# Kernel tuning notes

Hardware: AMD Instinct MI355X
Metric: run time of the kernel (lower is better)

Reference implementation:

```python
import jax, jax.numpy as jnp
import numpy as np

VOCAB = 50257
B, T, D = 32, 2048, 512


def setup_inputs() -> dict:
    key = jax.random.key(0)
    k1, k2, k3 = jax.random.split(key, 3)
    vector_sequence = jax.random.normal(k1, (B, T, D), dtype=jnp.float32)
    # lengths in [1, T] to match realistic sentence lengths (avoids 0/0 in y)
    sentence_length = jax.random.randint(k2, (B,), 1, T + 1, dtype=jnp.int32)
    word_sequence = jax.random.randint(k3, (B, T), 0, VOCAB, dtype=jnp.int32)
    # ParameterDict of scalars flattened to one vector, init = 1/num_of_vocab
    weights = jnp.ones((VOCAB,), dtype=jnp.float32) / VOCAB
    return {
        "vector_sequence": vector_sequence,
        "sentence_length": sentence_length,
        "word_sequence": word_sequence,
        "weights": weights,
    }


def reference(vector_sequence, sentence_length, word_sequence, weights):
    # mask out positions >= sentence_length (original zeroes them in place)
    mask = (jnp.arange(T)[None, :] < sentence_length[:, None]).astype(
        vector_sequence.dtype
    )  # [B, T]
    vs = vector_sequence * mask[:, :, None]  # [B, T, D]
    # y = sum_t vs / sum_t |vs|  (per batch, per dim)
    y = jnp.sum(vs, axis=1) / jnp.sum(jnp.abs(vs), axis=1)  # [B, D]
    # per-token scalar weight gather; padded positions are already zero in vs
    w = weights[word_sequence]  # [B, T]
    y_hat = jnp.sum(vs * w[:, :, None], axis=1)  # [B, D]
    return (y, y_hat)
```

## Files before the change

kernel.cpp:

```cpp
#include <hip/hip_runtime.h>

#define NB 32
#define NT 2048
#define ND 512
#define NDQ 128
#define NC 128
#define TC (NT / NC)

__global__ __launch_bounds__(128) void vu_partial_kernel(
    const float* __restrict__ vs,
    const int* __restrict__ slen,
    const int* __restrict__ wseq,
    const float* __restrict__ weights,
    float4* __restrict__ ps,
    float4* __restrict__ pa,
    float4* __restrict__ pw)
{
    const int c  = blockIdx.x;
    const int b  = blockIdx.y;
    const int dq = threadIdx.x;

    const int t0   = c * TC;
    const int len  = slen[b];
    const int tEnd = min(t0 + TC, len);
    if (t0 >= tEnd) return;

    __shared__ float w_lds[TC];
    if (threadIdx.x < TC) {
        const int t = t0 + threadIdx.x;
        w_lds[threadIdx.x] = (t < tEnd) ? weights[wseq[b * NT + t]] : 0.0f;
    }
    __syncthreads();

    float4 s  = make_float4(0.f, 0.f, 0.f, 0.f);
    float4 sa = make_float4(0.f, 0.f, 0.f, 0.f);
    float4 sw = make_float4(0.f, 0.f, 0.f, 0.f);

    const float4* __restrict__ vsq = (const float4*)vs + ((size_t)b * NT + t0) * NDQ + dq;
    const int n = tEnd - t0;
    #pragma unroll 4
    for (int i = 0; i < n; ++i) {
        const float4 v = vsq[(size_t)i * NDQ];
        const float  w = w_lds[i];
        s.x += v.x; s.y += v.y; s.z += v.z; s.w += v.w;
        sa.x += fabsf(v.x); sa.y += fabsf(v.y); sa.z += fabsf(v.z); sa.w += fabsf(v.w);
        sw.x = fmaf(v.x, w, sw.x); sw.y = fmaf(v.y, w, sw.y);
        sw.z = fmaf(v.z, w, sw.z); sw.w = fmaf(v.w, w, sw.w);
    }

    const size_t o = ((size_t)b * NC + c) * NDQ + dq;
    ps[o] = s;
    pa[o] = sa;
    pw[o] = sw;
}

__global__ __launch_bounds__(256) void vu_reduce_kernel(
    const float4* __restrict__ ps,
    const float4* __restrict__ pa,
    const float4* __restrict__ pw,
    const int* __restrict__ slen,
    float4* __restrict__ out)
{
    const int gid = blockIdx.x * 256 + threadIdx.x;
    if (gid >= NB * NDQ) return;
    const int b  = gid >> 7;
    const int dq = gid & (NDQ - 1);

    const int len  = slen[b];
    const int cEnd = (len + TC - 1) / TC;

    float4 s  = make_float4(0.f, 0.f, 0.f, 0.f);
    float4 sa = make_float4(0.f, 0.f, 0.f, 0.f);
    float4 sw = make_float4(0.f, 0.f, 0.f, 0.f);
    for (int c = 0; c < cEnd; ++c) {
        const size_t o = ((size_t)b * NC + c) * NDQ + dq;
        const float4 a = ps[o];
        const float4 x = pa[o];
        const float4 w = pw[o];
        s.x += a.x; s.y += a.y; s.z += a.z; s.w += a.w;
        sa.x += x.x; sa.y += x.y; sa.z += x.z; sa.w += x.w;
        sw.x += w.x; sw.y += w.y; sw.z += w.z; sw.w += w.w;
    }
    float4 y;
    y.x = s.x / sa.x; y.y = s.y / sa.y; y.z = s.z / sa.z; y.w = s.w / sa.w;
    out[(size_t)b * NDQ + dq] = y;
    out[(size_t)NB * NDQ + (size_t)b * NDQ + dq] = sw;
}

extern "C" void kernel_launch(void* const* d_in, const int* in_sizes, int n_in,
                              void* d_out, int out_size, void* d_ws, size_t ws_size,
                              hipStream_t stream) {
    const float* vs      = (const float*)d_in[0];
    const int*   slen    = (const int*)d_in[1];
    const int*   wseq    = (const int*)d_in[2];
    const float* weights = (const float*)d_in[3];
    float4*      out     = (float4*)d_out;

    const size_t stride = (size_t)NB * NC * NDQ;
    float4* ps = (float4*)d_ws;
    float4* pa = ps + stride;
    float4* pw = pa + stride;

    dim3 g1(NC, NB);
    vu_partial_kernel<<<g1, 128, 0, stream>>>(vs, slen, wseq, weights, ps, pa, pw);

    const int n2 = NB * NDQ;
    vu_reduce_kernel<<<(n2 + 255) / 256, 256, 0, stream>>>(ps, pa, pw, slen, out);
}
```

Measured before the change: 222.4 us.

## Replace partial-sum buffers with atomic accumulation and halve chunk count

The per-chunk partial sums are no longer written to a workspace and re-read by a reduction kernel. Each block now atomically adds its float results into small per-batch accumulators that are zeroed first with a memset, and the final kernel only divides and writes. The number of time chunks per batch drops from 128 to 64, which gives fewer blocks with longer loops and fewer atomics per address. The cost is an extra memset launch, atomic contention, nondeterministic float summation order, and possibly lower occupancy for streaming the large input.

Result: faster. 211.3 us (-5.0%).

```diff
diff --git a/kernel.cpp b/kernel.cpp
--- a/kernel.cpp
+++ b/kernel.cpp
@@ -4,7 +4,7 @@
 #define NT 2048
 #define ND 512
 #define NDQ 128
-#define NC 128
+#define NC 64
 #define TC (NT / NC)
 
 __global__ __launch_bounds__(128) void vu_partial_kernel(
@@ -12,9 +12,9 @@
     const int* __restrict__ slen,
     const int* __restrict__ wseq,
     const float* __restrict__ weights,
-    float4* __restrict__ ps,
-    float4* __restrict__ pa,
-    float4* __restrict__ pw)
+    float* __restrict__ accS,
+    float* __restrict__ accA,
+    float* __restrict__ accW)
 {
     const int c  = blockIdx.x;
     const int b  = blockIdx.y;
@@ -36,7 +36,8 @@
     float4 sa = make_float4(0.f, 0.f, 0.f, 0.f);
     float4 sw = make_float4(0.f, 0.f, 0.f, 0.f);
 
-    const float4* __restrict__ vsq = (const float4*)vs + ((size_t)b * NT + t0) * NDQ + dq;
+    const float4* __restrict__ vsq =
+        (const float4*)vs + ((size_t)b * NT + t0) * NDQ + dq;
     const int n = tEnd - t0;
     #pragma unroll 4
     for (int i = 0; i < n; ++i) {
@@ -48,43 +49,31 @@
         sw.z = fmaf(v.z, w, sw.z); sw.w = fmaf(v.w, w, sw.w);
     }
 
-    const size_t o = ((size_t)b * NC + c) * NDQ + dq;
-    ps[o] = s;
-    pa[o] = sa;
-    pw[o] = sw;
+    const size_t o = (size_t)b * ND + (size_t)dq * 4;
+    atomicAdd(&accS[o + 0], s.x);  atomicAdd(&accS[o + 1], s.y);
+    atomicAdd(&accS[o + 2], s.z);  atomicAdd(&accS[o + 3], s.w);
+    atomicAdd(&accA[o + 0], sa.x); atomicAdd(&accA[o + 1], sa.y);
+    atomicAdd(&accA[o + 2], sa.z); atomicAdd(&accA[o + 3], sa.w);
+    atomicAdd(&accW[o + 0], sw.x); atomicAdd(&accW[o + 1], sw.y);
+    atomicAdd(&accW[o + 2], sw.z); atomicAdd(&accW[o + 3], sw.w);
 }
 
-__global__ __launch_bounds__(256) void vu_reduce_kernel(
-    const float4* __restrict__ ps,
-    const float4* __restrict__ pa,
-    const float4* __restrict__ pw,
-    const int* __restrict__ slen,
+__global__ __launch_bounds__(256) void vu_final_kernel(
+    const float4* __restrict__ accS,
+    const float4* __restrict__ accA,
+    const float4* __restrict__ accW,
     float4* __restrict__ out)
 {
     const int gid = blockIdx.x * 256 + threadIdx.x;
     if (gid >= NB * NDQ) return;
-    const int b  = gid >> 7;
-    const int dq = gid & (NDQ - 1);
 
-    const int len  = slen[b];
-    const int cEnd = (len + TC - 1) / TC;
-
-    float4 s  = make_float4(0.f, 0.f, 0.f, 0.f);
-    float4 sa = make_float4(0.f, 0.f, 0.f, 0.f);
-    float4 sw = make_float4(0.f, 0.f, 0.f, 0.f);
-    for (int c = 0; c < cEnd; ++c) {
-        const size_t o = ((size_t)b * NC + c) * NDQ + dq;
-        const float4 a = ps[o];
-        const float4 x = pa[o];
-        const float4 w = pw[o];
-        s.x += a.x; s.y += a.y; s.z += a.z; s.w += a.w;
-        sa.x += x.x; sa.y += x.y; sa.z += x.z; sa.w += x.w;
-        sw.x += w.x; sw.y += w.y; sw.z += w.z; sw.w += w.w;
-    }
+    const float4 s  = accS[gid];
+    const float4 sa = accA[gid];
+    const float4 sw = accW[gid];
     float4 y;
     y.x = s.x / sa.x; y.y = s.y / sa.y; y.z = s.z / sa.z; y.w = s.w / sa.w;
-    out[(size_t)b * NDQ + dq] = y;
-    out[(size_t)NB * NDQ + (size_t)b * NDQ + dq] = sw;
+    out[gid] = y;
+    out[(size_t)NB * NDQ + gid] = sw;
 }
 
 extern "C" void kernel_launch(void* const* d_in, const int* in_sizes, int n_in,
@@ -96,14 +85,17 @@
     const float* weights = (const float*)d_in[3];
     float4*      out     = (float4*)d_out;
 
-    const size_t stride = (size_t)NB * NC * NDQ;
-    float4* ps = (float4*)d_ws;
-    float4* pa = ps + stride;
-    float4* pw = pa + stride;
+    float* accS = (float*)d_ws;
+    float* accA = accS + (size_t)NB * ND;
+    float* accW = accA + (size_t)NB * ND;
+
+    hipMemsetAsync(d_ws, 0, (size_t)3 * NB * ND * sizeof(float), stream);
 
     dim3 g1(NC, NB);
-    vu_partial_kernel<<<g1, 128, 0, stream>>>(vs, slen, wseq, weights, ps, pa, pw);
+    vu_partial_kernel<<<g1, 128, 0, stream>>>(vs, slen, wseq, weights,
+                                              accS, accA, accW);
 
     const int n2 = NB * NDQ;
-    vu_reduce_kernel<<<(n2 + 255) / 256, 256, 0, stream>>>(ps, pa, pw, slen, out);
+    vu_final_kernel<<<(n2 + 255) / 256, 256, 0, stream>>>(
+        (const float4*)accS, (const float4*)accA, (const float4*)accW, out);
 }
```
